# Optimization experiments

Measured on AMD Instinct MI355X. Metric: run time of the kernel, lower is better.

## Reference

```python
import jax, jax.numpy as jnp
import numpy as np

B, T, IN, HID, OUT = 64, 250, 1024, 2048, 256
TAU_TRACE = 20.0
TAU_MEM = 20.0
THR = 1.0
LR = 1e-4
WD = 0.01
DECAY_TRACE = float(np.exp(-1.0 / TAU_TRACE))
ALPHA = float(np.exp(-1.0 / TAU_MEM))


def _spike(v):
    # Heaviside spike with straight-through sigmoid surrogate gradient
    sur = jax.nn.sigmoid(4.0 * (v - THR))
    hard = (v > THR).astype(v.dtype)
    return sur + jax.lax.stop_gradient(hard - sur)


def _lif(current, v):
    # leaky integrate-and-fire with soft reset
    v = ALPHA * v + current
    z = _spike(v)
    v = v - z * THR
    return z, v


def _exp_convolve(spk, trace, decay):
    return decay * trace + (1.0 - decay) * spk


def _stdp(pre_trace, post_trace, w):
    # delta_w = lr * (batch-mean post x pre outer product - weight decay), detached
    outer = jnp.einsum('bo,bi->oi', post_trace, pre_trace) / pre_trace.shape[0]
    return jax.lax.stop_gradient(LR * (outer - WD * w))


def setup_inputs() -> dict:
    key = jax.random.key(0)
    k1, k2, k3 = jax.random.split(key, 3)
    x = (jax.random.uniform(k1, (B, T, IN)) < 0.1).astype(jnp.float32)  # spike raster
    input_weight = jax.random.uniform(k2, (HID, IN), dtype=jnp.float32)
    hidden_weight = jax.random.uniform(k3, (OUT, HID), dtype=jnp.float32)
    return {"x": x, "input_weight": input_weight, "hidden_weight": hidden_weight, "train": 1}


def reference(x, input_weight, hidden_weight, train):
    b = x.shape[0]
    dt = x.dtype
    v1 = jnp.zeros((b, HID), dt)
    v2 = jnp.zeros((b, OUT), dt)
    l1_tr = jnp.zeros((b, HID), dt)
    l2_tr = jnp.zeros((b, OUT), dt)
    in_tr = jnp.zeros((b, IN), dt)
    xs = jnp.swapaxes(x, 0, 1)  # [T, B, IN]

    if train:
        def step(carry, spk):
            w_in, w_hid, in_tr, l1_tr, l2_tr, v1, v2 = carry
            in_tr = _exp_convolve(spk, in_tr, DECAY_TRACE)
            l1, v1 = _lif(0.2 * (spk @ w_in.T), v1)
            l1_tr = _exp_convolve(l1, l1_tr, DECAY_TRACE)
            l2, v2 = _lif(0.2 * (l1 @ w_hid.T), v2)
            l2_tr = _exp_convolve(l2, l2_tr, DECAY_TRACE)
            w_in = w_in + _stdp(in_tr, l1_tr, w_in)
            w_hid = w_hid + _stdp(l1_tr, l2_tr, w_hid)
            return (w_in, w_hid, in_tr, l1_tr, l2_tr, v1, v2), (l1, l2)

        carry0 = (input_weight, hidden_weight, in_tr, l1_tr, l2_tr, v1, v2)
        carry, (l1s, l2s) = jax.lax.scan(step, carry0, xs)
        _, _, _, l1_tr, l2_tr, v1, v2 = carry
    else:
        def step(carry, spk):
            in_tr, v1, v2 = carry
            in_tr = _exp_convolve(spk, in_tr, DECAY_TRACE)
            l1, v1 = _lif(0.2 * (spk @ input_weight.T), v1)
            l2, v2 = _lif(0.2 * (l1 @ hidden_weight.T), v2)
            return (in_tr, v1, v2), (l1, l2)

        (_, v1, v2), (l1s, l2s) = jax.lax.scan(step, (in_tr, v1, v2), xs)

    l1_seq = jnp.swapaxes(l1s, 0, 1)  # [B, T, HID]
    l2_seq = jnp.swapaxes(l2s, 0, 1)  # [B, T, OUT]
    return l1_seq, l2_seq, v1, v2, l1_tr, l2_tr
```

## Files before the change

kernel.cpp:

```cpp
#include <hip/hip_runtime.h>
#include <hip/hip_cooperative_groups.h>
#include <stdint.h>

namespace cg = cooperative_groups;

#define BB   64
#define TTT  250
#define INN  1024
#define HIDD 2048
#define OUTT 256

#define DECAYF 0.951229424500714f
#define ALPHAF 0.951229424500714f
#define LRF    1e-4f
#define WDF    0.01f
#define SCLF   0.2f

#define O_L1SEQ 0
#define O_L2SEQ 32768000
#define O_V1    36864000
#define O_V2    36995072
#define O_L1TR  37011456
#define O_L2TR  37142528

#define CH  3
#define NPH 84

#define WS_XBITS 0
#define WS_INTRT 73728
#define WS_L1BIT 1253376
#define WS_L1TT  1351680
#define WS_FLAG  2924544

#define NB1 64
#define NB2 16
#define NBLK 80
#define NTHR 512

typedef __attribute__((ext_vector_type(8))) short short8v;
typedef __attribute__((ext_vector_type(4))) float float4v;

__device__ inline short f2bf(float f) {
  union { float f; uint32_t u; } c; c.f = f;
  uint32_t u = c.u + 0x7fffu + ((c.u >> 16) & 1u);
  return (short)(u >> 16);
}

__device__ inline short8v expand8(uint32_t byte) {
  union { uint32_t u[4]; short8v v; } r;
#pragma unroll
  for (int p2 = 0; p2 < 4; p2++) {
    r.u[p2] = (((byte >> (2 * p2)) & 1u) ? 0x3F80u : 0u) |
              (((byte >> (2 * p2 + 1)) & 1u) ? 0x3F800000u : 0u);
  }
  return r.v;
}

__device__ inline int ldf(int* p) {
  return __hip_atomic_load(p, __ATOMIC_RELAXED, __HIP_MEMORY_SCOPE_AGENT);
}
__device__ inline void postflag(int* p) {
  __hip_atomic_fetch_add(p, 1, __ATOMIC_RELEASE, __HIP_MEMORY_SCOPE_AGENT);
}

__device__ inline int swz1024(int row, int k) {
  return row * 1024 + ((((k) >> 3) ^ (row & 7)) << 3) + ((k) & 7);
}
__device__ inline int swz2048(int row, int k) {
  return row * 2048 + ((((k) >> 3) ^ (row & 7)) << 3) + ((k) & 7);
}
__device__ inline int swz64(int row, int k) {
  return row * 64 + ((((k) >> 3) ^ (row & 7)) << 3) + ((k) & 7);
}

struct SG1 {
  short winb[32 * 1024];
  float v1s[64 * 33];
  float l1trs[64 * 33];
  short l1trT[32 * 64];
  float red[2048];
};
struct SG2 {
  short whb[16 * 2048];
  float v2s[64 * 17];
  float l2trs[64 * 17];
  short l2trT[16 * 64];
  float red[4 * 256];
};

__global__ __launch_bounds__(NTHR, 1) void kmain(const float* __restrict__ x,
                                                 const float* __restrict__ w_in,
                                                 const float* __restrict__ w_hid,
                                                 float* __restrict__ out,
                                                 char* __restrict__ ws) {
  __shared__ __align__(16) char smem[94720];
  cg::grid_group grid = cg::this_grid();
  const int bid = blockIdx.x, tid = threadIdx.x;
  const int lane = tid & 63, wv = tid >> 6;
  const int mr = lane & 15, q = lane >> 4;

  int* FB = (int*)(ws + WS_FLAG);
  int* FP = FB;
  int* FE = FB + 128;
  int* FL2 = FB + 256;

  if (bid == 0) for (int c = tid; c < 384; c += NTHR) FB[c] = 0;
  grid.sync();

  if (bid < NB1) {
    SG1& S = *(SG1*)smem;
    const int h0 = bid * 32;
    const int btw = wv & 3, kh = wv >> 2;
    float wreg[64];
    const int ia = wv * 128 + lane, ib2 = ia + 64;
    float itra = 0.f, itrb = 0.f;

#pragma unroll
    for (int j = 0; j < 8; j++) {
      const int i = (wv * 8 + j) * 16 + mr;
#pragma unroll
      for (int ht2 = 0; ht2 < 2; ht2++)
#pragma unroll
        for (int r = 0; r < 4; r++) {
          const int hl = ht2 * 16 + q * 4 + r;
          float w = w_in[(h0 + hl) * INN + i];
          wreg[(j * 2 + ht2) * 4 + r] = w;
          S.winb[swz1024(hl, i)] = f2bf(w);
        }
    }
    for (int c = tid; c < 64 * 33; c += NTHR) { S.v1s[c] = 0.f; S.l1trs[c] = 0.f; }
    for (int s = 0; s < CH; s++) {
      float xa = x[(bid * TTT + s) * INN + ia];
      float xb2 = x[(bid * TTT + s) * INN + ib2];
      itra = DECAYF * itra + (1.f - DECAYF) * xa;
      itrb = DECAYF * itrb + (1.f - DECAYF) * xb2;
      short* intT = (short*)(ws + WS_INTRT) + s * (INN * BB);
      intT[ia * 64 + bid] = f2bf(itra);
      intT[ib2 * 64 + bid] = f2bf(itrb);
      unsigned long long balA = __ballot(xa > 0.5f);
      unsigned long long balB = __ballot(xb2 > 0.5f);
      if (lane == 0) {
        uint32_t* xbw = (uint32_t*)(ws + WS_XBITS) + s * (BB * 32) + bid * 32 + wv * 4;
        xbw[0] = (uint32_t)balA; xbw[1] = (uint32_t)(balA >> 32);
        xbw[2] = (uint32_t)balB; xbw[3] = (uint32_t)(balB >> 32);
      }
    }
    __syncthreads();
    if (tid == 0) postflag(&FP[0]);

    for (int p = 0; p < NPH; p++) {
      const int t0 = p * CH;
      const int ns = (TTT - t0 < CH) ? (TTT - t0) : CH;
      if (tid == 0) {
        for (;;) {
          int a = ldf(&FP[p]);
          int b2 = (p >= 2) ? ldf(&FE[p - 2]) : 64;
          int c2 = (p >= 2) ? ldf(&FL2[p - 2]) : 16;
          if (a >= 64 && b2 >= 64 && c2 >= 16) break;
        }
        __threadfence();
      }
      __syncthreads();

      for (int s = 0; s < ns; s++) {
        const int t = t0 + s;
        const uint32_t* xbw = (const uint32_t*)(ws + WS_XBITS) +
                              ((p % 3) * CH + s) * (BB * 32);
        float4v acc0 = {0.f, 0.f, 0.f, 0.f}, acc1 = acc0;
        {
          const uint32_t* brow = xbw + (btw * 16 + mr) * 32 + kh * 16;
#pragma unroll 8
          for (int ks = 0; ks < 16; ks++) {
            const int koff = ks * 32 + q * 8;
            short8v af = expand8(brow[ks] >> (q * 8));
            short8v bf0 = *(const short8v*)&S.winb[swz1024(mr, kh * 512 + koff)];
            short8v bf1 = *(const short8v*)&S.winb[swz1024(16 + mr, kh * 512 + koff)];
            acc0 = __builtin_amdgcn_mfma_f32_16x16x32_bf16(af, bf0, acc0, 0, 0, 0);
            acc1 = __builtin_amdgcn_mfma_f32_16x16x32_bf16(af, bf1, acc1, 0, 0, 0);
          }
        }
        if (kh == 1) {
          *(float4v*)&S.red[(btw * 2 + 0) * 256 + lane * 4] = acc0;
          *(float4v*)&S.red[(btw * 2 + 1) * 256 + lane * 4] = acc1;
        }
        __syncthreads();

        short* l1ttg = (short*)(ws + WS_L1TT) + ((p & 1) * CH + s) * (HIDD * BB);
        if (kh == 0) {
          const int b0 = btw * 16 + q * 4;
          float zf0[4], zf1[4];
#pragma unroll
          for (int ht2 = 0; ht2 < 2; ht2++) {
            float4v ac = ht2 ? acc1 : acc0;
            float4v o4 = *(const float4v*)&S.red[(btw * 2 + ht2) * 256 + lane * 4];
            const int hl = ht2 * 16 + mr, h = h0 + hl;
            short trs[4];
#pragma unroll
            for (int r = 0; r < 4; r++) {
              const int b = b0 + r;
              float v = ALPHAF * S.v1s[b * 33 + hl] + SCLF * (ac[r] + o4[r]);
              float z = v > 1.0f ? 1.0f : 0.0f;
              v -= z;
              S.v1s[b * 33 + hl] = v;
              out[O_L1SEQ + (b * TTT + t) * HIDD + h] = z;
              if (ht2 == 0) zf0[r] = z; else zf1[r] = z;
              float tr = DECAYF * S.l1trs[b * 33 + hl] + (1.f - DECAYF) * z;
              S.l1trs[b * 33 + hl] = tr;
              short tb = f2bf(tr);
              S.l1trT[swz64(hl, b)] = tb;
              trs[r] = tb;
            }
            *(short4*)(l1ttg + h * 64 + b0) = *(short4*)trs;
          }
          uint32_t* l1bw = (uint32_t*)(ws + WS_L1BIT) + ((p & 1) * CH + s) * (BB * 64);
#pragma unroll
          for (int r = 0; r < 4; r++) {
            unsigned long long bal0 = __ballot(zf0[r] > 0.5f);
            unsigned long long bal1 = __ballot(zf1[r] > 0.5f);
            if (mr == 0) {
              uint32_t w0 = (uint32_t)((bal0 >> (q * 16)) & 0xFFFFull);
              uint32_t w1 = (uint32_t)((bal1 >> (q * 16)) & 0xFFFFull);
              l1bw[(b0 + r) * 64 + bid] = w0 | (w1 << 16);
            }
          }
        }
        __syncthreads();

        {
          const short* intT = (const short*)(ws + WS_INTRT) + ((p % 3) * CH + s) * (INN * BB);
#pragma unroll
          for (int j = 0; j < 8; j++) {
            const int it = wv * 8 + j;
            float4v a20 = {0.f, 0.f, 0.f, 0.f}, a21 = a20;
#pragma unroll
            for (int ks = 0; ks < 2; ks++) {
              const int koff = ks * 32 + q * 8;
              short8v bf = *(const short8v*)(intT + (it * 16 + mr) * 64 + koff);
              short8v af0 = *(const short8v*)&S.l1trT[swz64(mr, koff)];
              short8v af1 = *(const short8v*)&S.l1trT[swz64(16 + mr, koff)];
              a20 = __builtin_amdgcn_mfma_f32_16x16x32_bf16(af0, bf, a20, 0, 0, 0);
              a21 = __builtin_amdgcn_mfma_f32_16x16x32_bf16(af1, bf, a21, 0, 0, 0);
            }
            const int i = it * 16 + mr;
#pragma unroll
            for (int ht2 = 0; ht2 < 2; ht2++) {
              float4v a2 = ht2 ? a21 : a20;
#pragma unroll
              for (int r = 0; r < 4; r++) {
                const int hl = ht2 * 16 + q * 4 + r;
                const int widx = (j * 2 + ht2) * 4 + r;
                float w = wreg[widx] * (1.f - LRF * WDF) + (LRF / 64.f) * a2[r];
                wreg[widx] = w;
                S.winb[swz1024(hl, i)] = f2bf(w);
              }
            }
          }
        }
        __syncthreads();

        if (s == 0 && p + 1 < NPH) {
          const int pt0 = (p + 1) * CH, pp = (p + 1) % 3;
          for (int s2 = 0; s2 < CH && pt0 + s2 < TTT; s2++) {
            float xa = x[(bid * TTT + pt0 + s2) * INN + ia];
            float xb2 = x[(bid * TTT + pt0 + s2) * INN + ib2];
            itra = DECAYF * itra + (1.f - DECAYF) * xa;
            itrb = DECAYF * itrb + (1.f - DECAYF) * xb2;
            short* intTn = (short*)(ws + WS_INTRT) + (pp * CH + s2) * (INN * BB);
            intTn[ia * 64 + bid] = f2bf(itra);
            intTn[ib2 * 64 + bid] = f2bf(itrb);
            unsigned long long balA = __ballot(xa > 0.5f);
            unsigned long long balB = __ballot(xb2 > 0.5f);
            if (lane == 0) {
              uint32_t* xbwn = (uint32_t*)(ws + WS_XBITS) + (pp * CH + s2) * (BB * 32) +
                               bid * 32 + wv * 4;
              xbwn[0] = (uint32_t)balA; xbwn[1] = (uint32_t)(balA >> 32);
              xbwn[2] = (uint32_t)balB; xbwn[3] = (uint32_t)(balB >> 32);
            }
          }
          __syncthreads();
          if (tid == 0) postflag(&FP[p + 1]);
        }
      }
      if (tid == 0) postflag(&FE[p]);
    }
    for (int c = tid; c < 64 * 32; c += NTHR) {
      const int b = c >> 5, hl = c & 31;
      out[O_V1 + b * HIDD + h0 + hl] = S.v1s[b * 33 + hl];
      out[O_L1TR + b * HIDD + h0 + hl] = S.l1trs[b * 33 + hl];
    }
  } else {
    SG2& S = *(SG2*)smem;
    const int o0 = (bid - NB1) * 16;
    const int bt = wv & 3, kh = wv >> 2;
    float wreg[64];

#pragma unroll
    for (int j = 0; j < 16; j++) {
      const int hcol = (wv * 16 + j) * 16 + mr;
#pragma unroll
      for (int r = 0; r < 4; r++) {
        const int ol = q * 4 + r;
        float w = w_hid[(o0 + ol) * HIDD + hcol];
        wreg[j * 4 + r] = w;
        S.whb[swz2048(ol, hcol)] = f2bf(w);
      }
    }
    for (int c = tid; c < 64 * 17; c += NTHR) { S.v2s[c] = 0.f; S.l2trs[c] = 0.f; }

    for (int p = 0; p < NPH; p++) {
      const int t0 = p * CH;
      const int ns = (TTT - t0 < CH) ? (TTT - t0) : CH;
      if (tid == 0) {
        while (ldf(&FE[p]) < 64) {}
        __threadfence();
      }
      __syncthreads();

      for (int s = 0; s < ns; s++) {
        const int u = t0 + s;
        const uint32_t* l1bw = (const uint32_t*)(ws + WS_L1BIT) +
                               ((p & 1) * CH + s) * (BB * 64);
        float4v acc = {0.f, 0.f, 0.f, 0.f};
        {
          const uint32_t* brow = l1bw + (bt * 16 + mr) * 64 + kh * 32;
#pragma unroll 8
          for (int ks = 0; ks < 32; ks++) {
            const int kk = kh * 1024 + ks * 32 + q * 8;
            short8v af = expand8(brow[ks] >> (q * 8));
            short8v bf = *(const short8v*)&S.whb[swz2048(mr, kk)];
            acc = __builtin_amdgcn_mfma_f32_16x16x32_bf16(af, bf, acc, 0, 0, 0);
          }
        }
        if (kh == 1) { *(float4v*)&S.red[bt * 256 + lane * 4] = acc; }
        __syncthreads();
        if (kh == 0) {
          float4v o4 = *(const float4v*)&S.red[bt * 256 + lane * 4];
#pragma unroll
          for (int r = 0; r < 4; r++) {
            const int b = bt * 16 + q * 4 + r;
            float v = ALPHAF * S.v2s[b * 17 + mr] + SCLF * (acc[r] + o4[r]);
            float z = v > 1.0f ? 1.0f : 0.0f;
            v -= z;
            S.v2s[b * 17 + mr] = v;
            out[O_L2SEQ + (b * TTT + u) * OUTT + o0 + mr] = z;
            float tr = DECAYF * S.l2trs[b * 17 + mr] + (1.f - DECAYF) * z;
            S.l2trs[b * 17 + mr] = tr;
            S.l2trT[swz64(mr, b)] = f2bf(tr);
          }
        }
        __syncthreads();

        {
          const short* l1ttg = (const short*)(ws + WS_L1TT) + ((p & 1) * CH + s) * (HIDD * BB);
#pragma unroll
          for (int j = 0; j < 16; j++) {
            const int htile = wv * 16 + j;
            float4v a2 = {0.f, 0.f, 0.f, 0.f};
#pragma unroll
            for (int ks = 0; ks < 2; ks++) {
              const int koff = ks * 32 + q * 8;
              short8v af = *(const short8v*)&S.l2trT[swz64(mr, koff)];
              short8v bf = *(const short8v*)(l1ttg + (htile * 16 + mr) * 64 + koff);
              a2 = __builtin_amdgcn_mfma_f32_16x16x32_bf16(af, bf, a2, 0, 0, 0);
            }
            const int hcol = htile * 16 + mr;
#pragma unroll
            for (int r = 0; r < 4; r++) {
              const int ol = q * 4 + r;
              float w = wreg[j * 4 + r] * (1.f - LRF * WDF) + (LRF / 64.f) * a2[r];
              wreg[j * 4 + r] = w;
              S.whb[swz2048(ol, hcol)] = f2bf(w);
            }
          }
        }
        __syncthreads();
      }
      if (tid == 0) postflag(&FL2[p]);
    }
    for (int c = tid; c < 64 * 16; c += NTHR) {
      const int b = c >> 4, ol = c & 15;
      out[O_V2 + b * OUTT + o0 + ol] = S.v2s[b * 17 + ol];
      out[O_L2TR + b * OUTT + o0 + ol] = S.l2trs[b * 17 + ol];
    }
  }
}

extern "C" void kernel_launch(void* const* d_in, const int* in_sizes, int n_in,
                              void* d_out, int out_size, void* d_ws, size_t ws_size,
                              hipStream_t stream) {
  const float* x = (const float*)d_in[0];
  const float* w_in = (const float*)d_in[1];
  const float* w_hid = (const float*)d_in[2];
  float* out = (float*)d_out;
  char* ws = (char*)d_ws;

  void* args[] = {(void*)&x, (void*)&w_in, (void*)&w_hid, (void*)&out, (void*)&ws};
  hipLaunchCooperativeKernel(reinterpret_cast<void*>(kmain), dim3(NBLK), dim3(NTHR),
                             args, 0, stream);
}
```

Measured before the change: 3.359 ms.

## Double chunk size, drop layer-1 split-K reduction, prefetch trace tiles, lighten barriers

Grows the time-step chunk per phase from 3 to 6, which halves the number of cross-block flag handshakes. Workspace offsets are enlarged to match. Layer-1 waves now split over hidden tiles instead of K halves, so the LDS reduction buffer and one barrier per step go away, and spike bits are written as 16-bit halves. Both layers prefetch the global trace tiles used by the STDP update into registers before the forward MFMA loop, and __syncthreads is replaced by a raw lgkmcnt-wait barrier. The layer-2 completion flag becomes a relaxed atomic. The costs are more register pressure and weaker memory-ordering guarantees, which could race.

```diff
diff --git a/kernel.cpp b/kernel.cpp
--- a/kernel.cpp
+++ b/kernel.cpp
@@ -23,14 +23,14 @@
 #define O_L1TR  37011456
 #define O_L2TR  37142528
 
-#define CH  3
-#define NPH 84
+#define CH  6
+#define NPH 42
 
 #define WS_XBITS 0
-#define WS_INTRT 73728
-#define WS_L1BIT 1253376
-#define WS_L1TT  1351680
-#define WS_FLAG  2924544
+#define WS_INTRT 147456
+#define WS_L1BIT 2506752
+#define WS_L1TT  2703360
+#define WS_FLAG  5849088
 
 #define NB1 64
 #define NB2 16
@@ -56,11 +56,18 @@
   return r.v;
 }
 
+__device__ inline void bar_lds() {
+  asm volatile("s_waitcnt lgkmcnt(0)\n\ts_barrier" ::: "memory");
+}
+
 __device__ inline int ldf(int* p) {
   return __hip_atomic_load(p, __ATOMIC_RELAXED, __HIP_MEMORY_SCOPE_AGENT);
 }
 __device__ inline void postflag(int* p) {
   __hip_atomic_fetch_add(p, 1, __ATOMIC_RELEASE, __HIP_MEMORY_SCOPE_AGENT);
+}
+__device__ inline void postflag_rx(int* p) {
+  __hip_atomic_fetch_add(p, 1, __ATOMIC_RELAXED, __HIP_MEMORY_SCOPE_AGENT);
 }
 
 __device__ inline int swz1024(int row, int k) {
@@ -78,7 +85,6 @@
   float v1s[64 * 33];
   float l1trs[64 * 33];
   short l1trT[32 * 64];
-  float red[2048];
 };
 struct SG2 {
   short whb[16 * 2048];
@@ -110,7 +116,7 @@
   if (bid < NB1) {
     SG1& S = *(SG1*)smem;
     const int h0 = bid * 32;
-    const int btw = wv & 3, kh = wv >> 2;
+    const int btw = wv & 3, htw = wv >> 2;
     float wreg[64];
     const int ia = wv * 128 + lane, ib2 = ia + 64;
     float itra = 0.f, itrb = 0.f;
@@ -129,7 +135,7 @@
         }
     }
     for (int c = tid; c < 64 * 33; c += NTHR) { S.v1s[c] = 0.f; S.l1trs[c] = 0.f; }
-    for (int s = 0; s < CH; s++) {
+    for (int s = 0; s < CH && s < TTT; s++) {
       float xa = x[(bid * TTT + s) * INN + ia];
       float xb2 = x[(bid * TTT + s) * INN + ib2];
       itra = DECAYF * itra + (1.f - DECAYF) * xa;
@@ -160,88 +166,75 @@
         }
         __threadfence();
       }
-      __syncthreads();
+      bar_lds();
 
       for (int s = 0; s < ns; s++) {
         const int t = t0 + s;
-        const uint32_t* xbw = (const uint32_t*)(ws + WS_XBITS) +
-                              ((p % 3) * CH + s) * (BB * 32);
-        float4v acc0 = {0.f, 0.f, 0.f, 0.f}, acc1 = acc0;
+        const short* intT = (const short*)(ws + WS_INTRT) + ((p % 3) * CH + s) * (INN * BB);
+        short8v pf[16];
+#pragma unroll
+        for (int j = 0; j < 8; j++)
+#pragma unroll
+          for (int ks = 0; ks < 2; ks++)
+            pf[j * 2 + ks] = *(const short8v*)(intT + ((wv * 8 + j) * 16 + mr) * 64 +
+                                               ks * 32 + q * 8);
+
+        const uint32_t* brow = (const uint32_t*)(ws + WS_XBITS) +
+                               ((p % 3) * CH + s) * (BB * 32) + (btw * 16 + mr) * 32;
+        float4v acc = {0.f, 0.f, 0.f, 0.f};
+#pragma unroll
+        for (int ks = 0; ks < 32; ks++) {
+          short8v af = expand8(brow[ks] >> (q * 8));
+          short8v bf = *(const short8v*)&S.winb[swz1024(htw * 16 + mr, ks * 32 + q * 8)];
+          acc = __builtin_amdgcn_mfma_f32_16x16x32_bf16(af, bf, acc, 0, 0, 0);
+        }
+
+        short* l1ttg = (short*)(ws + WS_L1TT) + ((p & 1) * CH + s) * (HIDD * BB);
+        unsigned short* l1bh = (unsigned short*)(ws + WS_L1BIT) +
+                               ((p & 1) * CH + s) * (BB * 128);
         {
-          const uint32_t* brow = xbw + (btw * 16 + mr) * 32 + kh * 16;
-#pragma unroll 8
-          for (int ks = 0; ks < 16; ks++) {
-            const int koff = ks * 32 + q * 8;
-            short8v af = expand8(brow[ks] >> (q * 8));
-            short8v bf0 = *(const short8v*)&S.winb[swz1024(mr, kh * 512 + koff)];
-            short8v bf1 = *(const short8v*)&S.winb[swz1024(16 + mr, kh * 512 + koff)];
-            acc0 = __builtin_amdgcn_mfma_f32_16x16x32_bf16(af, bf0, acc0, 0, 0, 0);
-            acc1 = __builtin_amdgcn_mfma_f32_16x16x32_bf16(af, bf1, acc1, 0, 0, 0);
-          }
-        }
-        if (kh == 1) {
-          *(float4v*)&S.red[(btw * 2 + 0) * 256 + lane * 4] = acc0;
-          *(float4v*)&S.red[(btw * 2 + 1) * 256 + lane * 4] = acc1;
-        }
-        __syncthreads();
-
-        short* l1ttg = (short*)(ws + WS_L1TT) + ((p & 1) * CH + s) * (HIDD * BB);
-        if (kh == 0) {
+          const int hl = htw * 16 + mr, h = h0 + hl;
           const int b0 = btw * 16 + q * 4;
-          float zf0[4], zf1[4];
-#pragma unroll
-          for (int ht2 = 0; ht2 < 2; ht2++) {
-            float4v ac = ht2 ? acc1 : acc0;
-            float4v o4 = *(const float4v*)&S.red[(btw * 2 + ht2) * 256 + lane * 4];
-            const int hl = ht2 * 16 + mr, h = h0 + hl;
-            short trs[4];
-#pragma unroll
-            for (int r = 0; r < 4; r++) {
-              const int b = b0 + r;
-              float v = ALPHAF * S.v1s[b * 33 + hl] + SCLF * (ac[r] + o4[r]);
-              float z = v > 1.0f ? 1.0f : 0.0f;
-              v -= z;
-              S.v1s[b * 33 + hl] = v;
-              out[O_L1SEQ + (b * TTT + t) * HIDD + h] = z;
-              if (ht2 == 0) zf0[r] = z; else zf1[r] = z;
-              float tr = DECAYF * S.l1trs[b * 33 + hl] + (1.f - DECAYF) * z;
-              S.l1trs[b * 33 + hl] = tr;
-              short tb = f2bf(tr);
-              S.l1trT[swz64(hl, b)] = tb;
-              trs[r] = tb;
-            }
-            *(short4*)(l1ttg + h * 64 + b0) = *(short4*)trs;
-          }
-          uint32_t* l1bw = (uint32_t*)(ws + WS_L1BIT) + ((p & 1) * CH + s) * (BB * 64);
+          short trs[4]; float zf[4];
 #pragma unroll
           for (int r = 0; r < 4; r++) {
-            unsigned long long bal0 = __ballot(zf0[r] > 0.5f);
-            unsigned long long bal1 = __ballot(zf1[r] > 0.5f);
-            if (mr == 0) {
-              uint32_t w0 = (uint32_t)((bal0 >> (q * 16)) & 0xFFFFull);
-              uint32_t w1 = (uint32_t)((bal1 >> (q * 16)) & 0xFFFFull);
-              l1bw[(b0 + r) * 64 + bid] = w0 | (w1 << 16);
-            }
-          }
-        }
-        __syncthreads();
+            const int b = b0 + r;
+            float v = ALPHAF * S.v1s[b * 33 + hl] + SCLF * acc[r];
+            float z = v > 1.0f ? 1.0f : 0.0f;
+            v -= z;
+            S.v1s[b * 33 + hl] = v;
+            out[O_L1SEQ + (b * TTT + t) * HIDD + h] = z;
+            zf[r] = z;
+            float tr = DECAYF * S.l1trs[b * 33 + hl] + (1.f - DECAYF) * z;
+            S.l1trs[b * 33 + hl] = tr;
+            short tb = f2bf(tr);
+            S.l1trT[swz64(hl, b)] = tb;
+            trs[r] = tb;
+          }
+          *(short4*)(l1ttg + h * 64 + b0) = *(short4*)trs;
+#pragma unroll
+          for (int r = 0; r < 4; r++) {
+            unsigned long long bal = __ballot(zf[r] > 0.5f);
+            if (mr == 0)
+              l1bh[(b0 + r) * 128 + bid * 2 + htw] =
+                  (unsigned short)((bal >> (q * 16)) & 0xFFFFull);
+          }
+        }
+        bar_lds();
 
         {
-          const short* intT = (const short*)(ws + WS_INTRT) + ((p % 3) * CH + s) * (INN * BB);
 #pragma unroll
           for (int j = 0; j < 8; j++) {
-            const int it = wv * 8 + j;
             float4v a20 = {0.f, 0.f, 0.f, 0.f}, a21 = a20;
 #pragma unroll
             for (int ks = 0; ks < 2; ks++) {
               const int koff = ks * 32 + q * 8;
-              short8v bf = *(const short8v*)(intT + (it * 16 + mr) * 64 + koff);
               short8v af0 = *(const short8v*)&S.l1trT[swz64(mr, koff)];
               short8v af1 = *(const short8v*)&S.l1trT[swz64(16 + mr, koff)];
-              a20 = __builtin_amdgcn_mfma_f32_16x16x32_bf16(af0, bf, a20, 0, 0, 0);
-              a21 = __builtin_amdgcn_mfma_f32_16x16x32_bf16(af1, bf, a21, 0, 0, 0);
-            }
-            const int i = it * 16 + mr;
+              a20 = __builtin_amdgcn_mfma_f32_16x16x32_bf16(af0, pf[j * 2 + ks], a20, 0, 0, 0);
+              a21 = __builtin_amdgcn_mfma_f32_16x16x32_bf16(af1, pf[j * 2 + ks], a21, 0, 0, 0);
+            }
+            const int i = (wv * 8 + j) * 16 + mr;
 #pragma unroll
             for (int ht2 = 0; ht2 < 2; ht2++) {
               float4v a2 = ht2 ? a21 : a20;
@@ -256,7 +249,7 @@
             }
           }
         }
-        __syncthreads();
+        bar_lds();
 
         if (s == 0 && p + 1 < NPH) {
           const int pt0 = (p + 1) * CH, pp = (p + 1) % 3;
@@ -281,6 +274,7 @@
           if (tid == 0) postflag(&FP[p + 1]);
         }
       }
+      __syncthreads();
       if (tid == 0) postflag(&FE[p]);
     }
     for (int c = tid; c < 64 * 32; c += NTHR) {
@@ -314,25 +308,31 @@
         while (ldf(&FE[p]) < 64) {}
         __threadfence();
       }
-      __syncthreads();
+      bar_lds();
 
       for (int s = 0; s < ns; s++) {
         const int u = t0 + s;
-        const uint32_t* l1bw = (const uint32_t*)(ws + WS_L1BIT) +
-                               ((p & 1) * CH + s) * (BB * 64);
+        const short* l1ttg = (const short*)(ws + WS_L1TT) + ((p & 1) * CH + s) * (HIDD * BB);
+        short8v pf[16];
+#pragma unroll
+        for (int j = 0; j < 8; j++)
+#pragma unroll
+          for (int ks = 0; ks < 2; ks++)
+            pf[j * 2 + ks] = *(const short8v*)(l1ttg + ((wv * 16 + j) * 16 + mr) * 64 +
+                                               ks * 32 + q * 8);
+
+        const uint32_t* brow = (const uint32_t*)(ws + WS_L1BIT) +
+                               ((p & 1) * CH + s) * (BB * 64) + (bt * 16 + mr) * 64 + kh * 32;
         float4v acc = {0.f, 0.f, 0.f, 0.f};
-        {
-          const uint32_t* brow = l1bw + (bt * 16 + mr) * 64 + kh * 32;
-#pragma unroll 8
-          for (int ks = 0; ks < 32; ks++) {
-            const int kk = kh * 1024 + ks * 32 + q * 8;
-            short8v af = expand8(brow[ks] >> (q * 8));
-            short8v bf = *(const short8v*)&S.whb[swz2048(mr, kk)];
-            acc = __builtin_amdgcn_mfma_f32_16x16x32_bf16(af, bf, acc, 0, 0, 0);
-          }
+#pragma unroll
+        for (int ks = 0; ks < 32; ks++) {
+          const int kk = kh * 1024 + ks * 32 + q * 8;
+          short8v af = expand8(brow[ks] >> (q * 8));
+          short8v bf = *(const short8v*)&S.whb[swz2048(mr, kk)];
+          acc = __builtin_amdgcn_mfma_f32_16x16x32_bf16(af, bf, acc, 0, 0, 0);
         }
         if (kh == 1) { *(float4v*)&S.red[bt * 256 + lane * 4] = acc; }
-        __syncthreads();
+        bar_lds();
         if (kh == 0) {
           float4v o4 = *(const float4v*)&S.red[bt * 256 + lane * 4];
 #pragma unroll
@@ -348,22 +348,19 @@
             S.l2trT[swz64(mr, b)] = f2bf(tr);
           }
         }
-        __syncthreads();
+        bar_lds();
 
         {
-          const short* l1ttg = (const short*)(ws + WS_L1TT) + ((p & 1) * CH + s) * (HIDD * BB);
-#pragma unroll
-          for (int j = 0; j < 16; j++) {
-            const int htile = wv * 16 + j;
+#pragma unroll
+          for (int j = 0; j < 8; j++) {
+            const int hcol = (wv * 16 + j) * 16 + mr;
             float4v a2 = {0.f, 0.f, 0.f, 0.f};
 #pragma unroll
             for (int ks = 0; ks < 2; ks++) {
               const int koff = ks * 32 + q * 8;
               short8v af = *(const short8v*)&S.l2trT[swz64(mr, koff)];
-              short8v bf = *(const short8v*)(l1ttg + (htile * 16 + mr) * 64 + koff);
-              a2 = __builtin_amdgcn_mfma_f32_16x16x32_bf16(af, bf, a2, 0, 0, 0);
-            }
-            const int hcol = htile * 16 + mr;
+              a2 = __builtin_amdgcn_mfma_f32_16x16x32_bf16(af, pf[j * 2 + ks], a2, 0, 0, 0);
+            }
 #pragma unroll
             for (int r = 0; r < 4; r++) {
               const int ol = q * 4 + r;
@@ -372,10 +369,30 @@
               S.whb[swz2048(ol, hcol)] = f2bf(w);
             }
           }
-        }
-        __syncthreads();
-      }
-      if (tid == 0) postflag(&FL2[p]);
+#pragma unroll
+          for (int j = 8; j < 16; j++) {
+            const int htile = wv * 16 + j;
+            const int hcol = htile * 16 + mr;
+            float4v a2 = {0.f, 0.f, 0.f, 0.f};
+#pragma unroll
+            for (int ks = 0; ks < 2; ks++) {
+              const int koff = ks * 32 + q * 8;
+              short8v bf = *(const short8v*)(l1ttg + (htile * 16 + mr) * 64 + koff);
+              short8v af = *(const short8v*)&S.l2trT[swz64(mr, koff)];
+              a2 = __builtin_amdgcn_mfma_f32_16x16x32_bf16(af, bf, a2, 0, 0, 0);
+            }
+#pragma unroll
+            for (int r = 0; r < 4; r++) {
+              const int ol = q * 4 + r;
+              float w = wreg[j * 4 + r] * (1.f - LRF * WDF) + (LRF / 64.f) * a2[r];
+              wreg[j * 4 + r] = w;
+              S.whb[swz2048(ol, hcol)] = f2bf(w);
+            }
+          }
+        }
+        bar_lds();
+      }
+      if (tid == 0) postflag_rx(&FL2[p]);
     }
     for (int c = tid; c < 64 * 16; c += NTHR) {
       const int b = c >> 4, ol = c & 15;
```

New measurement: 4.021 ms. 1.2x slower.
